# Kernel optimization log

Measured on AMD Instinct MI355X. Metric: run time of the kernel, lower is better.

## Reference

```python
import jax, jax.numpy as jnp
import numpy as np

L = 40   # seq_length (sentence includes root; sent_length = L-1)
B = 16   # batch
V = 10000  # vocab
F = 512  # feature_size = 2*hidden (bidirectional)
H = 256  # classifier hidden
NEG = -jnp.inf


def _mlp(x, W1, b1, W2, b2):
    # Classifier / BinaryClassifier: Linear -> tanh -> Linear
    return jnp.tanh(x @ W1 + b1) @ W2 + b2


def setup_inputs() -> dict:
    key = jax.random.key(0)
    ks = jax.random.split(key, 10)
    s = 0.05
    return {
        "h": jax.random.normal(ks[0], (L, B, F), jnp.float32),
        "sentence": jax.random.randint(ks[1], (L, B), 0, V),
        "Wt1": jax.random.normal(ks[2], (2 * F, H), jnp.float32) * s,
        "bt1": jnp.zeros((H,), jnp.float32),
        "Wt2": jax.random.normal(ks[3], (H, 1), jnp.float32) * s,
        "bt2": jnp.zeros((1,), jnp.float32),
        "Ww1": jax.random.normal(ks[4], (2 * F, H), jnp.float32) * s,
        "bw1": jnp.zeros((H,), jnp.float32),
        "Ww2": jax.random.normal(ks[5], (H, V), jnp.float32) * s,
        "bw2": jnp.zeros((V,), jnp.float32),
    }


def reference(h, sentence, Wt1, bt1, Wt2, bt2, Ww1, bw1, Ww2, bw2):
    sent_length = L - 1
    # all ordered pairs i < j (forward enumeration order of batch_feature_selection)
    iu, ju = np.triu_indices(L, k=1)          # [P]
    feat = jnp.concatenate([h[iu], h[ju]], axis=-1)   # [P, B, 2F]

    t_logit = _mlp(feat, Wt1, bt1, Wt2, bt2)[..., 0]  # [P, B]
    sh = jax.nn.log_sigmoid(-t_logit)                 # shift log-prob
    re = jax.nn.log_sigmoid(t_logit)                  # reduce log-prob

    # word model log-softmax, gathered at target token sentence[j+1]
    wl = _mlp(feat, Ww1, bw1, Ww2, bw2)               # [P, B, V]
    ju1 = np.minimum(ju + 1, L - 1)                   # pairs with j = L-1 are unused
    tgt = sentence[ju1]                               # [P, B]
    gathered = jnp.take_along_axis(wl, tgt[..., None], axis=-1)[..., 0]
    wlp = gathered - jax.nn.logsumexp(wl, axis=-1)    # [P, B]

    # dense [L, L, B] tables (only i<j entries used)
    SHW = jnp.full((L, L, B), NEG, jnp.float32).at[iu, ju].set(sh + wlp)  # word_prob_list
    RE = jnp.full((L, L, B), NEG, jnp.float32).at[iu, ju].set(re)

    # init cell: stack_next=False -> word prob of sentence[1] from features (0,0)
    feat0 = jnp.concatenate([h[0], h[0]], axis=-1)    # [B, 2F]
    lp0 = jax.nn.log_softmax(_mlp(feat0, Ww1, bw1, Ww2, bw2), axis=-1)
    init = jnp.take_along_axis(lp0, sentence[1][:, None], axis=1)[:, 0]  # [B]

    T = jnp.full((L, L, B), NEG, jnp.float32)
    T = T.at[0, 1].set(init)
    T = T.at[jnp.arange(1, sent_length), jnp.arange(2, sent_length + 1)].set(0.0)

    # CKY-style DP over span widths; each width is vectorized over start i and split k
    for gap in range(2, sent_length + 1):
        n_i = sent_length + 1 - gap
        i_arr = np.arange(n_i)
        j_arr = i_arr + gap
        k = i_arr[:, None] + np.arange(1, gap)[None, :]   # [n_i, gap-1]
        scores = (T[i_arr[:, None], k] + T[k, j_arr[:, None]]
                  + SHW[i_arr[:, None], k] + RE[k, j_arr[:, None]])  # [n_i, gap-1, B]
        T = T.at[i_arr, j_arr].set(jax.nn.logsumexp(scores, axis=1))

    # stack_next=False -> final_score = 0
    return T[0, sent_length]
```

## Files before the change

kernel.cpp:

```cpp
#include <hip/hip_runtime.h>
#include <hip/hip_bf16.h>

#define L_SEQ 40
#define B_SZ  16
#define V_SZ  10000
#define V_PAD 10240
#define NPAIR 780
#define NROWP 784
#define M_ROWS (NROWP * B_SZ)

typedef __attribute__((ext_vector_type(4))) float f32x4;
typedef __attribute__((ext_vector_type(4))) int   i32x4;
typedef __attribute__((ext_vector_type(8))) int   i32x8;

#if __has_builtin(__builtin_amdgcn_cvt_pk_fp8_f32)
__device__ __forceinline__ unsigned int pack4_fp8(float x0, float x1, float x2, float x3) {
    int lo = __builtin_amdgcn_cvt_pk_fp8_f32(x0, x1, 0, false);
    int full = __builtin_amdgcn_cvt_pk_fp8_f32(x2, x3, lo, true);
    return (unsigned int)full;
}
#else
__device__ __forceinline__ unsigned char f2e4m3(float f) {
    unsigned u = __float_as_uint(f);
    unsigned s = (u >> 24) & 0x80u;
    if ((u & 0x7FFFFFFFu) == 0) return (unsigned char)s;
    int E = (int)((u >> 23) & 0xFF) - 127 + 7;
    unsigned m = u & 0x7FFFFFu;
    if (E >= 16) return (unsigned char)(s | 0x7E);
    if (E >= 1) {
        unsigned keep = m >> 20, rest = m & 0xFFFFFu;
        keep += (rest > 0x80000u) || (rest == 0x80000u && (keep & 1));
        if (keep == 8) { keep = 0; E++; if (E >= 16) return (unsigned char)(s | 0x7E); }
        return (unsigned char)(s | (E << 3) | keep);
    }
    int shift = 1 - E;
    if (shift > 10) return (unsigned char)s;
    unsigned full = 0x800000u | m;
    unsigned sh = 20 + shift;
    unsigned keep = full >> sh, rem = full & ((1u << sh) - 1), half = 1u << (sh - 1);
    keep += (rem > half) || (rem == half && (keep & 1));
    if (keep >= 8) return (unsigned char)(s | (1 << 3));
    return (unsigned char)(s | keep);
}
__device__ __forceinline__ unsigned int pack4_fp8(float x0, float x1, float x2, float x3) {
    return (unsigned int)f2e4m3(x0) | ((unsigned int)f2e4m3(x1) << 8)
         | ((unsigned int)f2e4m3(x2) << 16) | ((unsigned int)f2e4m3(x3) << 24);
}
#endif

#if __has_builtin(__builtin_amdgcn_exp2f)
__device__ __forceinline__ float exp2_hw(float x) { return __builtin_amdgcn_exp2f(x); }
#else
__device__ __forceinline__ float exp2_hw(float x) { return __expf(x * 0.6931471805599453f); }
#endif

#if __has_builtin(__builtin_amdgcn_rcpf)
__device__ __forceinline__ float rcp_hw(float x) { return __builtin_amdgcn_rcpf(x); }
#else
__device__ __forceinline__ float rcp_hw(float x) { return 1.0f / x; }
#endif

__device__ __forceinline__ float fast_tanh(float x) {
    float e = exp2_hw(x * 2.885390081777926814f);
    return fmaf(-2.0f, rcp_hw(e + 1.0f), 1.0f);
}


__global__ __launch_bounds__(256) void prep_kernel(
        const float* __restrict__ Ww2, float* __restrict__ WwT,
        unsigned char* __restrict__ WbT,
        const float* __restrict__ h, const float* __restrict__ Wt1,
        const float* __restrict__ Ww1, float* __restrict__ UV) {
    const int bx = blockIdx.x;
    const int t = threadIdx.x;
    __shared__ float smem[32 * 132];
    if (bx < 640) {
        float (*tile)[132] = (float (*)[132])smem;
        int v0 = (bx % 80) * 128;
        int k0 = (bx / 80) * 32;
        int tx4 = t & 31, ky = t >> 5;
        int v = v0 + tx4 * 4;
#pragma unroll
        for (int r = 0; r < 4; r++) {
            int k = k0 + ky + r * 8;
            float4 val = make_float4(0.f, 0.f, 0.f, 0.f);
            if (v < V_SZ) val = *(const float4*)(Ww2 + (size_t)k * V_SZ + v);
            *(float4*)(&tile[ky + r * 8][tx4 * 4]) = val;
        }
        __syncthreads();
        int kx4 = t & 7, vr8 = t >> 3;
#pragma unroll
        for (int pass = 0; pass < 4; pass++) {
            int vr = vr8 + pass * 32;
            float c0 = tile[kx4 * 4 + 0][vr];
            float c1 = tile[kx4 * 4 + 1][vr];
            float c2 = tile[kx4 * 4 + 2][vr];
            float c3 = tile[kx4 * 4 + 3][vr];
            float4 cv = make_float4(c0, c1, c2, c3);
            *(float4*)(WwT + (size_t)(v0 + vr) * 256 + k0 + kx4 * 4) = cv;
            ((unsigned int*)WbT)[(size_t)(v0 + vr) * 64 + (k0 >> 2) + kx4] =
                pack4_fp8(c0, c1, c2, c3);
        }
    } else {
        float* hs = smem;
        int ub = bx - 640;
        int which = ub / 320;
        int rem = ub - which * 320;
        int m0 = (rem >> 2) * 8;
        int ks = rem & 3;
        int f0 = ks * 128;
        {
            int r = t >> 5, fq = t & 31;
            ((float4*)hs)[r * 32 + fq] =
                *(const float4*)(h + (size_t)(m0 + r) * 512 + f0 + fq * 4);
        }
        __syncthreads();
        const float* W = ((which < 2) ? Wt1 : Ww1)
                       + ((which & 1) ? 512 * 256 : 0) + (size_t)f0 * 256;
        float acc[8] = {};
        for (int f = 0; f < 128; f += 4) {
            float w0 = W[(f + 0) * 256 + t];
            float w1 = W[(f + 1) * 256 + t];
            float w2 = W[(f + 2) * 256 + t];
            float w3 = W[(f + 3) * 256 + t];
#pragma unroll
            for (int r = 0; r < 8; r++) {
                float4 hv = *(const float4*)(hs + r * 128 + f);
                acc[r] += hv.x * w0 + hv.y * w1 + hv.z * w2 + hv.w * w3;
            }
        }
        float* dst = UV + ((size_t)which * 640 + m0) * 256;
#pragma unroll
        for (int r = 0; r < 8; r++) atomicAdd(&dst[r * 256 + t], acc[r]);
    }
}

__global__ void build_rows(const float* __restrict__ UV,
                           const int* __restrict__ sentence,
                           const float* __restrict__ bt1,
                           const float* __restrict__ bw1,
                           const float* __restrict__ Wt2,
                           const float* __restrict__ bt2,
                           const float* __restrict__ WwT,
                           const float* __restrict__ bw2,
                           unsigned char* __restrict__ X,
                           float* __restrict__ tlog,
                           float* __restrict__ glog) {
    int w = blockIdx.x * 4 + (threadIdx.x >> 6);
    int lane = threadIdx.x & 63;
    int p = w >> 4, b = w & 15;
    int i = 0, j = 0;
    if (p < NPAIR) {
        int rem = p, len = L_SEQ - 1;
        while (rem >= len) { rem -= len; len--; i++; }
        j = i + 1 + rem;
    }
    int j1 = (j + 1 < L_SEQ) ? j + 1 : L_SEQ - 1;
    int tgt = sentence[j1 * B_SZ + b];
    const float4 ut = ((const float4*)(UV + 0 * 640 * 256 + (i * B_SZ + b) * 256))[lane];
    const float4 vt = ((const float4*)(UV + 1 * 640 * 256 + (j * B_SZ + b) * 256))[lane];
    const float4 uw = ((const float4*)(UV + 2 * 640 * 256 + (i * B_SZ + b) * 256))[lane];
    const float4 vw = ((const float4*)(UV + 3 * 640 * 256 + (j * B_SZ + b) * 256))[lane];
    const float4 bt = ((const float4*)bt1)[lane];
    const float4 bw = ((const float4*)bw1)[lane];
    const float4 w2 = ((const float4*)Wt2)[lane];
    const float4 wc = ((const float4*)(WwT + (size_t)tgt * 256))[lane];
    float xt0 = fast_tanh(ut.x + vt.x + bt.x), xt1 = fast_tanh(ut.y + vt.y + bt.y);
    float xt2 = fast_tanh(ut.z + vt.z + bt.z), xt3 = fast_tanh(ut.w + vt.w + bt.w);
    float xw0 = fast_tanh(uw.x + vw.x + bw.x), xw1 = fast_tanh(uw.y + vw.y + bw.y);
    float xw2 = fast_tanh(uw.z + vw.z + bw.z), xw3 = fast_tanh(uw.w + vw.w + bw.w);
    ((unsigned int*)X)[w * 64 + lane] = pack4_fp8(xw0, xw1, xw2, xw3);
    float td = xt0 * w2.x + xt1 * w2.y + xt2 * w2.z + xt3 * w2.w;
    float gd = xw0 * wc.x + xw1 * wc.y + xw2 * wc.z + xw3 * wc.w;
#pragma unroll
    for (int off = 32; off >= 1; off >>= 1) {
        td += __shfl_xor(td, off);
        gd += __shfl_xor(gd, off);
    }
    if (lane == 0) {
        tlog[w] = td + bt2[0];
        glog[w] = gd + bw2[tgt];
    }
}

#define RD8(BASE, KB, BR) \
    BR[0] = *(const i32x4*)((BASE) + offs[(KB)*8 + 0]); \
    BR[1] = *(const i32x4*)((BASE) + offs[(KB)*8 + 1]); \
    BR[2] = *(const i32x4*)((BASE) + offs[(KB)*8 + 2]); \
    BR[3] = *(const i32x4*)((BASE) + offs[(KB)*8 + 3]); \
    BR[4] = *(const i32x4*)((BASE) + offs[(KB)*8 + 4]); \
    BR[5] = *(const i32x4*)((BASE) + offs[(KB)*8 + 5]); \
    BR[6] = *(const i32x4*)((BASE) + offs[(KB)*8 + 6]); \
    BR[7] = *(const i32x4*)((BASE) + offs[(KB)*8 + 7]);

#define MF4(KB, NI, BR) { \
    i32x8 bv_ = __builtin_shufflevector(BR[2*(NI)], BR[2*(NI)+1], 0,1,2,3,4,5,6,7); \
    acc[0][NI] = __builtin_amdgcn_mfma_scale_f32_16x16x128_f8f6f4( \
        apan[0][KB], bv_, acc[0][NI], 0,0, 0,0x7F7F7F7F, 0,0x7F7F7F7F); \
    acc[1][NI] = __builtin_amdgcn_mfma_scale_f32_16x16x128_f8f6f4( \
        apan[1][KB], bv_, acc[1][NI], 0,0, 0,0x7F7F7F7F, 0,0x7F7F7F7F); \
    acc[2][NI] = __builtin_amdgcn_mfma_scale_f32_16x16x128_f8f6f4( \
        apan[2][KB], bv_, acc[2][NI], 0,0, 0,0x7F7F7F7F, 0,0x7F7F7F7F); \
    acc[3][NI] = __builtin_amdgcn_mfma_scale_f32_16x16x128_f8f6f4( \
        apan[3][KB], bv_, acc[3][NI], 0,0, 0,0x7F7F7F7F, 0,0x7F7F7F7F); \
}

#define EPI(NI) { \
    float bL_ = bl[NI]; \
    _Pragma("unroll") \
    for (int mi_ = 0; mi_ < 4; mi_++) \
        _Pragma("unroll") \
        for (int r_ = 0; r_ < 4; r_++) \
            PS[mi_][r_] += exp2_hw(fmaf(acc[mi_][NI][r_], L2E, bL_)); \
}

__global__ __launch_bounds__(512, 2) void big_gemm(
        const unsigned char* __restrict__ X,
        const unsigned char* __restrict__ WbT,
        const float* __restrict__ bw2,
        float* __restrict__ rowsum) {
    __shared__ unsigned char Bs[4][128 * 256];
    __shared__ float biasL[2048];
    const int t = threadIdx.x;
    const int wid = t >> 6, lane = t & 63;
    const int l15 = lane & 15, l4 = lane >> 4;
    const int rg = wid >> 1, ch = wid & 1;
    const int g = blockIdx.x;
    const int row0 = blockIdx.y * 256 + rg * 64;
    const int NIT = 16;
    const float L2E = 1.44269504088896340736f;

#pragma unroll
    for (int k = 0; k < 4; k++) {
        int idx = k * 512 + t;
        int col = g * 2048 + idx;
        biasL[idx] = (col < V_SZ) ? bw2[col] * L2E : -__builtin_inff();
    }

    int offs[16];
#pragma unroll
    for (int kb = 0; kb < 2; kb++)
#pragma unroll
        for (int ni = 0; ni < 4; ni++)
#pragma unroll
            for (int gg = 0; gg < 2; gg++) {
                int cc = ch * 64 + ni * 16 + l15;
                int gr = kb * 8 + l4 * 2 + gg;
                offs[kb * 8 + ni * 2 + gg] = cc * 256 + ((gr ^ (cc & 15)) << 4);
            }

    auto dmaB = [&](int buf, int it) {
        const unsigned char* Bg = WbT + (size_t)(g * 2048 + it * 128) * 256;
#pragma unroll
        for (int q = 0; q < 4; q++) {
            int off = (wid * 4 + q) * 1024;
            int F = off + lane * 16;
            int cc = F >> 8;
            int s = (F >> 4) & 15;
            int srcg = s ^ (cc & 15);
            __builtin_amdgcn_global_load_lds(
                (const __attribute__((address_space(1))) unsigned int*)(Bg + cc * 256 + (srcg << 4)),
                (__attribute__((address_space(3))) unsigned int*)(&Bs[buf][0] + off),
                16, 0, 0);
        }
    };

    i32x8 apan[4][2];
    {
        const unsigned char* Ag = X + (size_t)row0 * 256;
#pragma unroll
        for (int mi = 0; mi < 4; mi++)
#pragma unroll
            for (int kb = 0; kb < 2; kb++)
                apan[mi][kb] = *(const i32x8*)(Ag + (mi * 16 + l15) * 256 + kb * 128 + l4 * 32);
    }
    __builtin_amdgcn_sched_barrier(0);
    dmaB(0, 0);
    dmaB(1, 1);
    dmaB(2, 2);
    asm volatile("s_waitcnt vmcnt(12) lgkmcnt(0)" ::: "memory");
    __builtin_amdgcn_s_barrier();

    float PS[4][4] = {};

#pragma unroll 1
    for (int it = 0; it < NIT; it++) {
        if (it < NIT - 2)       asm volatile("s_waitcnt vmcnt(8)" ::: "memory");
        else if (it == NIT - 2) asm volatile("s_waitcnt vmcnt(4)" ::: "memory");
        else                    asm volatile("s_waitcnt vmcnt(0)" ::: "memory");
        __builtin_amdgcn_s_barrier();
        if (it + 3 < NIT) dmaB((it + 3) & 3, it + 3);
        const unsigned char* bufC = &Bs[it & 3][0];
        float bl[4];
#pragma unroll
        for (int ni = 0; ni < 4; ni++)
            bl[ni] = biasL[it * 128 + ch * 64 + ni * 16 + l15];
        f32x4 acc[4][4] = {};
        i32x4 br[8];
        __builtin_amdgcn_s_setprio(1);
        RD8(bufC, 0, br);
        MF4(0, 0, br); MF4(0, 1, br); MF4(0, 2, br); MF4(0, 3, br);
        RD8(bufC, 1, br);
        MF4(1, 0, br);
        MF4(1, 1, br); EPI(0);
        MF4(1, 2, br); EPI(1);
        MF4(1, 3, br); EPI(2);
        __builtin_amdgcn_s_setprio(0);
        EPI(3);
    }
#pragma unroll
    for (int mi = 0; mi < 4; mi++)
#pragma unroll
        for (int r = 0; r < 4; r++) {
            float v = PS[mi][r];
            v += __shfl_xor(v, 1); v += __shfl_xor(v, 2);
            v += __shfl_xor(v, 4); v += __shfl_xor(v, 8);
            if (l15 == 0)
                atomicAdd(&rowsum[row0 + mi * 16 + l4 * 4 + r], v);
        }
}

__global__ __launch_bounds__(1024) void dp_kernel(const float* __restrict__ tlog,
                          const float* __restrict__ glog,
                          const float* __restrict__ rowsum,
                          float* __restrict__ out) {
    __shared__ float Tl[1600], SHWl[1600], REl[1600];
    const int t = threadIdx.x;
    const int b = blockIdx.x;
    const float NEGINF = -__builtin_inff();
    for (int idx = t; idx < 1600; idx += 1024) {
        Tl[idx] = NEGINF; SHWl[idx] = NEGINF; REl[idx] = NEGINF;
    }
    __syncthreads();
    for (int p = t; p < NPAIR; p += 1024) {
        int i = 0, rem = p, len = L_SEQ - 1;
        while (rem >= len) { rem -= len; len--; i++; }
        int j = i + 1 + rem;
        int row = p * 16 + b;
        float tl = tlog[row];
        float re_v = (tl >= 0.f) ? -log1pf(__expf(-tl)) : (tl - log1pf(__expf(tl)));
        float sh_v = (tl <= 0.f) ? -log1pf(__expf(tl)) : (-tl - log1pf(__expf(-tl)));
        float wlp = glog[row] - __logf(rowsum[row]);
        SHWl[i * 40 + j] = sh_v + wlp;
        REl[i * 40 + j] = re_v;
    }
    if (t == 0) {
        int row = NPAIR * 16 + b;
        Tl[0 * 40 + 1] = glog[row] - __logf(rowsum[row]);
    }
    if (t >= 1 && t <= 38) Tl[t * 40 + t + 1] = 0.f;
    __syncthreads();
    const int tg = t >> 4, li = t & 15;
    for (int gap = 2; gap <= L_SEQ - 1; gap++) {
        int n_i = L_SEQ - gap;
        float m = NEGINF, s = 0.f;
        int i = tg, j = tg + gap;
        if (tg < n_i) {
            for (int k = i + 1 + li; k < j; k += 16) {
                float v = Tl[i * 40 + k] + Tl[k * 40 + j]
                        + SHWl[i * 40 + k] + REl[k * 40 + j];
                if (v > m) { s = s * __expf(m - v) + 1.f; m = v; }
                else s += __expf(v - m);
            }
        }
#pragma unroll
        for (int off = 1; off < 16; off <<= 1) {
            float mo = __shfl_xor(m, off), so = __shfl_xor(s, off);
            float M = fmaxf(m, mo);
            float sn = 0.f;
            if (m > NEGINF) sn += s * __expf(m - M);
            if (mo > NEGINF) sn += so * __expf(mo - M);
            m = M; s = sn;
        }
        if (tg < n_i && li == 0) Tl[i * 40 + j] = m + __logf(s);
        __syncthreads();
    }
    if (t == 0) out[b] = Tl[39];
}

extern "C" void kernel_launch(void* const* d_in, const int* in_sizes, int n_in,
                              void* d_out, int out_size, void* d_ws, size_t ws_size,
                              hipStream_t stream) {
    const float* h        = (const float*)d_in[0];
    const int*   sentence = (const int*)d_in[1];
    const float* Wt1      = (const float*)d_in[2];
    const float* bt1      = (const float*)d_in[3];
    const float* Wt2      = (const float*)d_in[4];
    const float* bt2      = (const float*)d_in[5];
    const float* Ww1      = (const float*)d_in[6];
    const float* bw1      = (const float*)d_in[7];
    const float* Ww2      = (const float*)d_in[8];
    const float* bw2      = (const float*)d_in[9];
    float* out = (float*)d_out;

    char* ws = (char*)d_ws;
    size_t off = 0;
    float* UV = (float*)(ws + off);                    off += 4ull * 640 * 256 * 4;
    unsigned char* X = (unsigned char*)(ws + off);     off += (size_t)M_ROWS * 256;
    unsigned char* WbT = (unsigned char*)(ws + off);   off += (size_t)V_PAD * 256;
    float* WwT = (float*)(ws + off);                   off += (size_t)V_PAD * 256 * 4;
    float* rowsum = (float*)(ws + off);                off += (size_t)M_ROWS * 4;
    float* tlog = (float*)(ws + off);                  off += (size_t)M_ROWS * 4;
    float* glog = (float*)(ws + off);                  off += (size_t)M_ROWS * 4;

    hipMemsetAsync(rowsum, 0, (size_t)M_ROWS * 4, stream);
    hipMemsetAsync(UV, 0, 4ull * 640 * 256 * 4, stream);
    prep_kernel<<<1920, 256, 0, stream>>>(Ww2, WwT, WbT, h, Wt1, Ww1, UV);
    build_rows<<<M_ROWS / 4, 256, 0, stream>>>(UV, sentence, bt1, bw1, Wt2, bt2,
                                               WwT, bw2, X, tlog, glog);
    big_gemm<<<dim3(5, 49), 512, 0, stream>>>(X, WbT, bw2, rowsum);
    dp_kernel<<<16, 1024, 0, stream>>>(tlog, glog, rowsum, out);
}
```

Baseline: 184.5 us.

## Run CKY DP with a single wavefront per batch, dropping block barriers

The DP kernel moves from 1024 threads per batch element to one 64-lane wavefront. Each gap iteration splits the lanes adaptively between span starts and split points, so the per-gap __syncthreads is replaced by an LDS wait plus a scheduling barrier. This removes 38 block-wide barriers across 16 waves. In exchange, each thread covers more of the table initialisation and pair loading, and early gaps with many starts get fewer lanes per span. Correctness depends on LDS ordering within one wavefront.

```diff
diff --git a/kernel.cpp b/kernel.cpp
--- a/kernel.cpp
+++ b/kernel.cpp
@@ -320,19 +320,18 @@
         }
 }
 
-__global__ __launch_bounds__(1024) void dp_kernel(const float* __restrict__ tlog,
+__global__ __launch_bounds__(64) void dp_kernel(const float* __restrict__ tlog,
                           const float* __restrict__ glog,
                           const float* __restrict__ rowsum,
                           float* __restrict__ out) {
     __shared__ float Tl[1600], SHWl[1600], REl[1600];
-    const int t = threadIdx.x;
+    const int lane = threadIdx.x;
     const int b = blockIdx.x;
     const float NEGINF = -__builtin_inff();
-    for (int idx = t; idx < 1600; idx += 1024) {
+    for (int idx = lane; idx < 1600; idx += 64) {
         Tl[idx] = NEGINF; SHWl[idx] = NEGINF; REl[idx] = NEGINF;
     }
-    __syncthreads();
-    for (int p = t; p < NPAIR; p += 1024) {
+    for (int p = lane; p < NPAIR; p += 64) {
         int i = 0, rem = p, len = L_SEQ - 1;
         while (rem >= len) { rem -= len; len--; i++; }
         int j = i + 1 + rem;
@@ -344,27 +343,31 @@
         SHWl[i * 40 + j] = sh_v + wlp;
         REl[i * 40 + j] = re_v;
     }
-    if (t == 0) {
+    if (lane == 0) {
         int row = NPAIR * 16 + b;
         Tl[0 * 40 + 1] = glog[row] - __logf(rowsum[row]);
     }
-    if (t >= 1 && t <= 38) Tl[t * 40 + t + 1] = 0.f;
-    __syncthreads();
-    const int tg = t >> 4, li = t & 15;
+    if (lane >= 1 && lane <= 38) Tl[lane * 40 + lane + 1] = 0.f;
+    asm volatile("s_waitcnt lgkmcnt(0)" ::: "memory");
+    __builtin_amdgcn_sched_barrier(0);
+
     for (int gap = 2; gap <= L_SEQ - 1; gap++) {
         int n_i = L_SEQ - gap;
+        int P = 64, lp = 6;
+        while (P > 1 && P * n_i > 64) { P >>= 1; lp--; }
+        int c = lane >> lp;
+        int s0 = lane & (P - 1);
         float m = NEGINF, s = 0.f;
-        int i = tg, j = tg + gap;
-        if (tg < n_i) {
-            for (int k = i + 1 + li; k < j; k += 16) {
+        if (c < n_i) {
+            int i = c, j = c + gap;
+            for (int k = i + 1 + s0; k < j; k += P) {
                 float v = Tl[i * 40 + k] + Tl[k * 40 + j]
                         + SHWl[i * 40 + k] + REl[k * 40 + j];
                 if (v > m) { s = s * __expf(m - v) + 1.f; m = v; }
                 else s += __expf(v - m);
             }
         }
-#pragma unroll
-        for (int off = 1; off < 16; off <<= 1) {
+        for (int off = 1; off < P; off <<= 1) {
             float mo = __shfl_xor(m, off), so = __shfl_xor(s, off);
             float M = fmaxf(m, mo);
             float sn = 0.f;
@@ -372,10 +375,11 @@
             if (mo > NEGINF) sn += so * __expf(mo - M);
             m = M; s = sn;
         }
-        if (tg < n_i && li == 0) Tl[i * 40 + j] = m + __logf(s);
-        __syncthreads();
-    }
-    if (t == 0) out[b] = Tl[39];
+        if (c < n_i && s0 == 0) Tl[c * 40 + c + gap] = m + __logf(s);
+        asm volatile("s_waitcnt lgkmcnt(0)" ::: "memory");
+        __builtin_amdgcn_sched_barrier(0);
+    }
+    if (lane == 0) out[b] = Tl[39];
 }
 
 extern "C" void kernel_launch(void* const* d_in, const int* in_sizes, int n_in,
@@ -409,5 +413,5 @@
     build_rows<<<M_ROWS / 4, 256, 0, stream>>>(UV, sentence, bt1, bw1, Wt2, bt2,
                                                WwT, bw2, X, tlog, glog);
     big_gemm<<<dim3(5, 49), 512, 0, stream>>>(X, WbT, bw2, rowsum);
-    dp_kernel<<<16, 1024, 0, stream>>>(tlog, glog, rowsum, out);
-}
+    dp_kernel<<<16, 64, 0, stream>>>(tlog, glog, rowsum, out);
+}
```

Result: slower. 219.0 us (+18.7%).
